# Kernel optimization log

Measured on AMD Instinct MI355X. Metric: run time of the kernel, lower is better.

The kernel has to match this reference:

```python
import jax, jax.numpy as jnp
import numpy as np

N = 25000   # nodes of type 'window'
E = 200000  # edges per relation
H = 512     # hidden_channels
OUT = 250   # out_channels
L = 4       # num_layers
R = 3       # relations: near, close, sim


def setup_inputs() -> dict:
    key = jax.random.key(0)
    ks = jax.random.split(key, 8)
    s = 1.0 / np.sqrt(H).astype(np.float32)
    x = jax.random.normal(ks[0], (N, H), jnp.float32)
    W_pre = jax.random.normal(ks[1], (H, H), jnp.float32) * s
    W_post = jax.random.normal(ks[2], (H, H), jnp.float32) * s
    Wl = jax.random.normal(ks[3], (L, R, H, H), jnp.float32) * s   # SAGEConv lin_l (neighbors)
    Wr = jax.random.normal(ks[4], (L, R, H, H), jnp.float32) * s   # SAGEConv lin_r (root)
    bl = jnp.zeros((L, R, H), jnp.float32)                         # lin_l bias
    W_out = jax.random.normal(ks[5], (H, OUT), jnp.float32) * s
    b_out = jnp.zeros((OUT,), jnp.float32)
    edges = jax.random.randint(ks[6], (R, 2, E), 0, N, jnp.int32)  # [rel, (src,dst), E]
    return dict(x=x, W_pre=W_pre, W_post=W_post, Wl=Wl, Wr=Wr, bl=bl,
                W_out=W_out, b_out=b_out, edges=edges)


def _leaky(v):
    return jnp.where(v >= 0, v, 0.2 * v)


def reference(x, W_pre, W_post, Wl, Wr, bl, W_out, b_out, edges):
    # pretransform + post_transform: leaky(leaky(x @ Wpre) @ Wpost)
    h = _leaky(_leaky(x @ W_pre) @ W_post)

    # per-relation destination in-degree (constant across layers)
    inv_deg = []
    for r in range(R):
        cnt = jax.ops.segment_sum(jnp.ones((E,), h.dtype), edges[r, 1], num_segments=N)
        inv_deg.append(1.0 / jnp.maximum(cnt, 1.0))  # [N]

    for l in range(L):
        acc = jnp.zeros_like(h)
        for r in range(R):
            src, dst = edges[r, 0], edges[r, 1]
            # mean aggregation of neighbor features over destinations
            agg = jax.ops.segment_sum(h[src], dst, num_segments=N) * inv_deg[r][:, None]
            # SAGEConv: lin_l(agg) + lin_r(x_root)
            acc = acc + (agg @ Wl[l, r] + bl[l, r] + h @ Wr[l, r])
        # HeteroConv aggr='mean' across relations, then LeakyReLU(0.2)
        h = _leaky(acc / R)

    return h @ W_out + b_out
```

## Files before the change

kernel.cpp:

```cpp
#include <hip/hip_runtime.h>

#define N_ 25000
#define E_ 200000
#define H_ 512
#define OUT_ 250
#define WSZ (H_ * H_)

typedef unsigned short u16;
typedef unsigned int u32;
typedef __bf16 bf16x8 __attribute__((ext_vector_type(8)));
typedef float f32x4 __attribute__((ext_vector_type(4)));

__device__ __forceinline__ u16 f2b(float f) {
  union { float f; u32 u; } c; c.f = f;
  u32 r = c.u + 0x7FFFu + ((c.u >> 16) & 1u);
  return (u16)(r >> 16);
}
__device__ __forceinline__ void async16(const void* g, void* l) {
  __builtin_amdgcn_global_load_lds((__attribute__((address_space(1))) void*)g,
                                   (__attribute__((address_space(3))) void*)l, 16, 0, 0);
}

__global__ void conv_hist(const float* __restrict__ x, u16* __restrict__ xb,
                          const int* __restrict__ edges, int* __restrict__ counts) {
  const int i = blockIdx.x * 256 + threadIdx.x;
  if (i < 3 * E_) {
    int r = i / E_, e = i - r * E_;
    int dst = edges[r * 2 * E_ + E_ + e];
    atomicAdd(&counts[r * N_ + dst], 1);
  }
  if (i < N_ * 512 / 4) {
    const float4 v = *(const float4*)(x + (size_t)i * 4);
    ushort4 o;
    o.x = f2b(v.x); o.y = f2b(v.y); o.z = f2b(v.z); o.w = f2b(v.w);
    *(ushort4*)(xb + (size_t)i * 4) = o;
  }
}

__global__ void prep_all(const float* __restrict__ Wpre, const float* __restrict__ Wpost,
                         const float* __restrict__ Wl, const float* __restrict__ Wr,
                         const float* __restrict__ Wout, const float* __restrict__ bl,
                         const float* __restrict__ bout,
                         u16* __restrict__ WT, u16* __restrict__ WoutT,
                         float* __restrict__ blSum, float* __restrict__ bOutF) {
  __shared__ u16 tile[32][33];
  const int id = blockIdx.z;
  const int tx = blockIdx.x, ty = blockIdx.y;
  const int x = threadIdx.x, y = threadIdx.y;
  if (id == 19) {
    if (tx || ty) return;
    const int t = y * 32 + x;
    for (int t0 = t; t0 < 512; t0 += 256) {
      for (int l = 0; l < 4; ++l)
        blSum[l * 512 + t0] = bl[(l * 3 + 0) * 512 + t0] + bl[(l * 3 + 1) * 512 + t0] +
                              bl[(l * 3 + 2) * 512 + t0];
    }
    if (t < 256) bOutF[t] = (t < OUT_) ? bout[t] : 0.0f;
    return;
  }
  if (id == 18) {
    if (tx >= 8) return;
#pragma unroll
    for (int i = 0; i < 4; ++i) {
      int row = ty * 32 + y + i * 8;
      int col = tx * 32 + x;
      tile[y + i * 8][x] = (col < OUT_) ? f2b(Wout[(size_t)row * OUT_ + col]) : (u16)0;
    }
    __syncthreads();
#pragma unroll
    for (int i = 0; i < 4; ++i)
      WoutT[(tx * 32 + y + i * 8) * 512 + ty * 32 + x] = tile[x][y + i * 8];
    return;
  }
  const float* src = nullptr;
  bool sum3 = false;
  if (id == 0) src = Wpre;
  else if (id == 1) src = Wpost;
  else {
    int li = (id - 2) >> 2, ri = (id - 2) & 3;
    if (ri < 3) src = Wl + (size_t)(li * 3 + ri) * WSZ;
    else { sum3 = true; src = Wr + (size_t)(li * 3) * WSZ; }
  }
#pragma unroll
  for (int i = 0; i < 4; ++i) {
    int row = ty * 32 + y + i * 8;
    int col = tx * 32 + x;
    float f = src[(size_t)row * 512 + col];
    if (sum3) f += src[WSZ + (size_t)row * 512 + col] + src[2 * WSZ + (size_t)row * 512 + col];
    tile[y + i * 8][x] = f2b(f);
  }
  __syncthreads();
#pragma unroll
  for (int i = 0; i < 4; ++i)
    WT[(size_t)id * WSZ + (tx * 32 + y + i * 8) * 512 + ty * 32 + x] = tile[x][y + i * 8];
}

__global__ __launch_bounds__(1024) void scan_kernel(const int* __restrict__ counts,
                                                    int* __restrict__ rowptr,
                                                    int* __restrict__ cursor,
                                                    float* __restrict__ invdeg) {
  const int r = blockIdx.x;
  const int* cnt = counts + r * N_;
  int* rp = rowptr + r * (N_ + 1);
  int* cur = cursor + r * N_;
  __shared__ int wsum[2][16];
  const int tid = threadIdx.x;
  const int wv = tid >> 6, lane = tid & 63;
  int roff = 0;
  int par = 0;
  for (int base = 0; base < N_; base += 1024, par ^= 1) {
    int v = (base + tid < N_) ? cnt[base + tid] : 0;
    int inc = v;
#pragma unroll
    for (int d = 1; d < 64; d <<= 1) {
      int t = __shfl_up(inc, d, 64);
      if (lane >= d) inc += t;
    }
    if (lane == 63) wsum[par][wv] = inc;
    __syncthreads();
    if (tid < 16) {
      int s = wsum[par][tid];
#pragma unroll
      for (int d = 1; d < 16; d <<= 1) {
        int t = __shfl_up(s, d, 64);
        if (tid >= d) s += t;
      }
      wsum[par][tid] = s;
    }
    __syncthreads();
    int woff = (wv == 0) ? 0 : wsum[par][wv - 1];
    int excl = roff + woff + inc - v;
    if (base + tid < N_) {
      rp[base + tid] = excl; cur[base + tid] = excl;
      invdeg[r * N_ + base + tid] = 1.0f / fmaxf((float)v, 1.0f);
    }
    roff += wsum[par][15];
  }
  if (tid == 0) rp[N_] = roff;
}

__global__ void scatter_kernel(const int* __restrict__ edges, int* __restrict__ cursor,
                               int* __restrict__ colidx) {
  int idx = blockIdx.x * 256 + threadIdx.x;
  if (idx >= 3 * E_) return;
  int r = idx / E_, e = idx - r * E_;
  int src = edges[r * 2 * E_ + e];
  int dst = edges[r * 2 * E_ + E_ + e];
  int pos = atomicAdd(&cursor[r * N_ + dst], 1);
  colidx[r * E_ + pos] = src;
}

__device__ __forceinline__ void acc8(float* acc, uint4 u) {
  union { u32 u; float f; } c;
  c.u = u.x << 16;          acc[0] += c.f;
  c.u = u.x & 0xffff0000u;  acc[1] += c.f;
  c.u = u.y << 16;          acc[2] += c.f;
  c.u = u.y & 0xffff0000u;  acc[3] += c.f;
  c.u = u.z << 16;          acc[4] += c.f;
  c.u = u.z & 0xffff0000u;  acc[5] += c.f;
  c.u = u.w << 16;          acc[6] += c.f;
  c.u = u.w & 0xffff0000u;  acc[7] += c.f;
}

__global__ __launch_bounds__(256) void agg_kernel(const u16* __restrict__ h,
                                                  const int* __restrict__ rowptr,
                                                  const int* __restrict__ colidx,
                                                  const float* __restrict__ invdeg,
                                                  u16* __restrict__ agg) {
  const int chunk = blockIdx.x & 7;
  const int nb = blockIdx.x >> 3;
  const int r = blockIdx.y;
  const int wv = threadIdx.x >> 6;
  const int lane = threadIdx.x & 63;
  const int grp = lane >> 3, sub = lane & 7;
  const int node = nb * 32 + wv * 8 + grp;
  if (node >= N_) return;
  const int* rp = rowptr + r * (N_ + 1);
  const int* ci = colidx + r * E_;
  const u16* hb = h + chunk * 64 + sub * 8;
  const int s = rp[node], e = rp[node + 1];
  float acc[8] = {0.f, 0.f, 0.f, 0.f, 0.f, 0.f, 0.f, 0.f};
  int p = s;
  for (; p + 4 <= e; p += 4) {
    int s0 = ci[p], s1 = ci[p + 1], s2 = ci[p + 2], s3 = ci[p + 3];
    uint4 u0 = *(const uint4*)(hb + (size_t)s0 * 512);
    uint4 u1 = *(const uint4*)(hb + (size_t)s1 * 512);
    uint4 u2 = *(const uint4*)(hb + (size_t)s2 * 512);
    uint4 u3 = *(const uint4*)(hb + (size_t)s3 * 512);
    acc8(acc, u0); acc8(acc, u1); acc8(acc, u2); acc8(acc, u3);
  }
  for (; p < e; ++p) acc8(acc, *(const uint4*)(hb + (size_t)ci[p] * 512));
  const float sc = invdeg[r * N_ + node];
  uint4 o;
  o.x = (u32)f2b(acc[0] * sc) | ((u32)f2b(acc[1] * sc) << 16);
  o.y = (u32)f2b(acc[2] * sc) | ((u32)f2b(acc[3] * sc) << 16);
  o.z = (u32)f2b(acc[4] * sc) | ((u32)f2b(acc[5] * sc) << 16);
  o.w = (u32)f2b(acc[6] * sc) | ((u32)f2b(acc[7] * sc) << 16);
  *(uint4*)(agg + ((size_t)r * N_ + node) * 512 + chunk * 64 + sub * 8) = o;
}

#define BM 128
#define BN 128
#define BK 64
#define CSTRIDE 136
__global__ __launch_bounds__(256, 4) void gemm_mfma(
    const u16* __restrict__ A0, const u16* __restrict__ A1,
    const u16* __restrict__ A2, const u16* __restrict__ A3,
    const u16* __restrict__ Bt, const float* __restrict__ bias,
    u16* __restrict__ C, float* __restrict__ Cf,
    int M, int G, int ldc, int Nreal, float scale, int leaky) {
  __shared__ __align__(16) u16 shmem[BM * CSTRIDE];
  u16* As = shmem;
  u16* Bs = shmem + BM * BK;
  const int tid = threadIdx.x;
  const int lane = tid & 63;
  const int w = tid >> 6;

  const int gx = gridDim.x;
  const int lin = blockIdx.y * gx + blockIdx.x;
  const int gsz = gx * 8;
  const int grp = lin / gsz;
  const int l = lin - grp * gsz;
  const int rem = (int)gridDim.y - grp * 8;
  int by, bx;
  if (rem >= 8) { by = grp * 8 + (l & 7); bx = l >> 3; }
  else          { by = grp * 8 + l % rem; bx = l / rem; }
  const int row0 = by * BM;
  const int col0 = bx * BN;

  int aOff[4], bOff[4], lOff[4];
#pragma unroll
  for (int i = 0; i < 4; ++i) {
    const int idx = i * 256 + tid;
    const int arow = idx >> 3;
    const int c = (idx & 7) ^ (arow & 7);
    int grow = row0 + arow; if (grow >= M) grow = M - 1;
    aOff[i] = grow * 512 + c * 8;
    bOff[i] = (col0 + arow) * 512 + c * 8;
    lOff[i] = idx * 16;
  }

  const int lm = lane & 15;
  const int lk = lane >> 4;
  const int x0 = ((lk ^ (lane & 7)) << 3);
  const int x1 = (((4 + lk) ^ (lane & 7)) << 3);
  const int wm = (w >> 1) * 64;
  const int wn = (w & 1) * 64;
  int aRow[4], bRow[4];
#pragma unroll
  for (int i = 0; i < 4; ++i) {
    aRow[i] = (wm + i * 16 + lm) * BK;
    bRow[i] = (wn + i * 16 + lm) * BK;
  }

  f32x4 acc[4][4] = {};

  for (int g = 0; g < G; ++g) {
    const u16* Ag = (g == 0) ? A0 : (g == 1) ? A1 : (g == 2) ? A2 : A3;
    const u16* Bg = Bt + ((size_t)g << 18);
#pragma unroll
    for (int ki = 0; ki < 8; ++ki) {
      const u16* Ab = Ag + ki * 64;
      const u16* Bb = Bg + ki * 64;
#pragma unroll
      for (int i = 0; i < 4; ++i) {
        async16(Ab + aOff[i], (char*)As + lOff[i]);
        async16(Bb + bOff[i], (char*)Bs + lOff[i]);
      }
      __syncthreads();
      {
        bf16x8 af[4], bfr[4];
#pragma unroll
        for (int i = 0; i < 4; ++i) {
          af[i]  = *(const bf16x8*)((const char*)As + ((aRow[i] + x0) << 1));
          bfr[i] = *(const bf16x8*)((const char*)Bs + ((bRow[i] + x0) << 1));
        }
#pragma unroll
        for (int i = 0; i < 4; ++i)
#pragma unroll
          for (int j = 0; j < 4; ++j)
            acc[i][j] = __builtin_amdgcn_mfma_f32_16x16x32_bf16(af[i], bfr[j], acc[i][j], 0, 0, 0);
#pragma unroll
        for (int i = 0; i < 4; ++i) {
          af[i]  = *(const bf16x8*)((const char*)As + ((aRow[i] + x1) << 1));
          bfr[i] = *(const bf16x8*)((const char*)Bs + ((bRow[i] + x1) << 1));
        }
#pragma unroll
        for (int i = 0; i < 4; ++i)
#pragma unroll
          for (int j = 0; j < 4; ++j)
            acc[i][j] = __builtin_amdgcn_mfma_f32_16x16x32_bf16(af[i], bfr[j], acc[i][j], 0, 0, 0);
      }
      __syncthreads();
    }
  }

  if (Cf) {
    const int crow_base = row0 + wm + (lk << 2);
    const int ccol_base = col0 + wn + lm;
#pragma unroll
    for (int i = 0; i < 4; ++i) {
#pragma unroll
      for (int j = 0; j < 4; ++j) {
        const int ccol = ccol_base + j * 16;
        const float badd = bias ? bias[ccol] : 0.0f;
#pragma unroll
        for (int rg = 0; rg < 4; ++rg) {
          const int crow = crow_base + i * 16 + rg;
          if (crow < M && ccol < Nreal) {
            float v = (acc[i][j][rg] + badd) * scale;
            if (leaky) v = (v >= 0.0f) ? v : 0.2f * v;
            Cf[(size_t)crow * ldc + ccol] = v;
          }
        }
      }
    }
    return;
  }
  {
    const int lrow_base = wm + (lk << 2);
    const int lcol_base = wn + lm;
#pragma unroll
    for (int i = 0; i < 4; ++i) {
#pragma unroll
      for (int j = 0; j < 4; ++j) {
        const int lcol = lcol_base + j * 16;
        const float badd = bias ? bias[col0 + lcol] : 0.0f;
#pragma unroll
        for (int rg = 0; rg < 4; ++rg) {
          const int lrow = lrow_base + i * 16 + rg;
          float v = (acc[i][j][rg] + badd) * scale;
          if (leaky) v = (v >= 0.0f) ? v : 0.2f * v;
          shmem[lrow * CSTRIDE + lcol] = f2b(v);
        }
      }
    }
    __syncthreads();
    const int rr = tid >> 4;
    const int c8 = (tid & 15) * 8;
#pragma unroll
    for (int pass = 0; pass < 8; ++pass) {
      const int r = pass * 16 + rr;
      const int crow = row0 + r;
      if (crow < M) {
        uint4 v = *(const uint4*)&shmem[r * CSTRIDE + c8];
        *(uint4*)(C + (size_t)crow * ldc + col0 + c8) = v;
      }
    }
  }
}

extern "C" void kernel_launch(void* const* d_in, const int* in_sizes, int n_in,
                              void* d_out, int out_size, void* d_ws, size_t ws_size,
                              hipStream_t stream) {
  const float* x     = (const float*)d_in[0];
  const float* Wpre  = (const float*)d_in[1];
  const float* Wpost = (const float*)d_in[2];
  const float* Wl    = (const float*)d_in[3];
  const float* Wr    = (const float*)d_in[4];
  const float* bl    = (const float*)d_in[5];
  const float* Wout  = (const float*)d_in[6];
  const float* bout  = (const float*)d_in[7];
  const int*   edges = (const int*)d_in[8];
  float* out = (float*)d_out;

  char* p = (char*)d_ws;
  auto alloc = [&](size_t b) { void* q = (void*)p; p += (b + 255) & ~(size_t)255; return q; };
  u16*   WT     = (u16*)alloc((size_t)18 * WSZ * 2);
  u16*   WoutT  = (u16*)alloc((size_t)256 * 512 * 2);
  float* blSum  = (float*)alloc(4 * 512 * 4);
  float* bOutF  = (float*)alloc(256 * 4);
  u16*   hA     = (u16*)alloc((size_t)N_ * 512 * 2);
  u16*   hB     = (u16*)alloc((size_t)N_ * 512 * 2);
  u16*   aggb   = (u16*)alloc((size_t)3 * N_ * 512 * 2);
  int*   counts = (int*)alloc(3 * N_ * 4);
  float* invdeg = (float*)alloc(3 * N_ * 4);
  int*   rowptr = (int*)alloc(3 * (N_ + 1) * 4);
  int*   cursor = (int*)alloc(3 * N_ * 4);
  int*   colidx = (int*)alloc((size_t)3 * E_ * 4);
  u16*   xb     = aggb;

  hipMemsetAsync(counts, 0, 3 * N_ * 4, stream);
  conv_hist<<<(N_ * 512 / 4 + 255) / 256, 256, 0, stream>>>(x, xb, edges, counts);
  prep_all<<<dim3(16, 16, 20), dim3(32, 8), 0, stream>>>(Wpre, Wpost, Wl, Wr, Wout, bl, bout,
                                                          WT, WoutT, blSum, bOutF);
  scan_kernel<<<3, 1024, 0, stream>>>(counts, rowptr, cursor, invdeg);
  scatter_kernel<<<(3 * E_ + 255) / 256, 256, 0, stream>>>(edges, cursor, colidx);

  const dim3 blk(256);
  const dim3 g512(512 / BN, (N_ + BM - 1) / BM);
  const dim3 gagg(((N_ + 31) / 32) * 8, 3);
  gemm_mfma<<<g512, blk, 0, stream>>>(xb, xb, xb, xb, WT, nullptr, hA, nullptr,
                                      N_, 1, 512, 512, 1.0f, 1);
  gemm_mfma<<<g512, blk, 0, stream>>>(hA, hA, hA, hA, WT + WSZ, nullptr, hB, nullptr,
                                      N_, 1, 512, 512, 1.0f, 1);

  u16* hc = hB; u16* hn = hA;
  for (int l = 0; l < 4; ++l) {
    agg_kernel<<<gagg, blk, 0, stream>>>(hc, rowptr, colidx, invdeg, aggb);
    gemm_mfma<<<g512, blk, 0, stream>>>(aggb, aggb + (size_t)N_ * 512, aggb + (size_t)2 * N_ * 512, hc,
                                        WT + (size_t)(2 + 4 * l) * WSZ, blSum + l * 512, hn, nullptr,
                                        N_, 4, 512, 512, 1.0f / 3.0f, 1);
    u16* t = hc; hc = hn; hn = t;
  }
  const dim3 gout(256 / BN, (N_ + BM - 1) / BM);
  gemm_mfma<<<gout, blk, 0, stream>>>(hc, hc, hc, hc, WoutT, bOutF, nullptr, out,
                                      N_, 1, OUT_, OUT_, 1.0f, 0);
}
```

Before: 792.2 us.

## Make aggregation persistent with per-XCC work queues and XCC-pinned column slices

The neighbor-aggregation kernel becomes a persistent kernel of 2048 blocks. Each block reads its hardware XCC id and uses it to pick which 64-column slice of h it gathers, so each die's L2 only ever holds one slice of the feature matrix. Node tiles for all three relations are handed out through a per-XCC atomic counter, one counter set per layer, to balance uneven in-degree work. This adds an atomic and two barriers per tile. Correctness relies on every XCC id 0–7 getting at least one block; if that fails, some column slices are never computed.

New measurement: 1.538 ms. +94.2%, slower.

```diff
diff --git a/kernel.cpp b/kernel.cpp
--- a/kernel.cpp
+++ b/kernel.cpp
@@ -162,41 +162,55 @@
   c.u = u.w & 0xffff0000u;  acc[7] += c.f;
 }
 
+#define AGG_TILES 782
+#define AGG_NT (AGG_TILES * 3)
 __global__ __launch_bounds__(256) void agg_kernel(const u16* __restrict__ h,
                                                   const int* __restrict__ rowptr,
                                                   const int* __restrict__ colidx,
                                                   const float* __restrict__ invdeg,
-                                                  u16* __restrict__ agg) {
-  const int chunk = blockIdx.x & 7;
-  const int nb = blockIdx.x >> 3;
-  const int r = blockIdx.y;
+                                                  u16* __restrict__ agg,
+                                                  int* __restrict__ wq) {
+  __shared__ int s_tile;
+  u32 xcc;
+  asm volatile("s_getreg_b32 %0, hwreg(HW_REG_XCC_ID)" : "=s"(xcc));
+  const int chunk = xcc & 7;
   const int wv = threadIdx.x >> 6;
   const int lane = threadIdx.x & 63;
   const int grp = lane >> 3, sub = lane & 7;
-  const int node = nb * 32 + wv * 8 + grp;
-  if (node >= N_) return;
-  const int* rp = rowptr + r * (N_ + 1);
-  const int* ci = colidx + r * E_;
   const u16* hb = h + chunk * 64 + sub * 8;
-  const int s = rp[node], e = rp[node + 1];
-  float acc[8] = {0.f, 0.f, 0.f, 0.f, 0.f, 0.f, 0.f, 0.f};
-  int p = s;
-  for (; p + 4 <= e; p += 4) {
-    int s0 = ci[p], s1 = ci[p + 1], s2 = ci[p + 2], s3 = ci[p + 3];
-    uint4 u0 = *(const uint4*)(hb + (size_t)s0 * 512);
-    uint4 u1 = *(const uint4*)(hb + (size_t)s1 * 512);
-    uint4 u2 = *(const uint4*)(hb + (size_t)s2 * 512);
-    uint4 u3 = *(const uint4*)(hb + (size_t)s3 * 512);
-    acc8(acc, u0); acc8(acc, u1); acc8(acc, u2); acc8(acc, u3);
-  }
-  for (; p < e; ++p) acc8(acc, *(const uint4*)(hb + (size_t)ci[p] * 512));
-  const float sc = invdeg[r * N_ + node];
-  uint4 o;
-  o.x = (u32)f2b(acc[0] * sc) | ((u32)f2b(acc[1] * sc) << 16);
-  o.y = (u32)f2b(acc[2] * sc) | ((u32)f2b(acc[3] * sc) << 16);
-  o.z = (u32)f2b(acc[4] * sc) | ((u32)f2b(acc[5] * sc) << 16);
-  o.w = (u32)f2b(acc[6] * sc) | ((u32)f2b(acc[7] * sc) << 16);
-  *(uint4*)(agg + ((size_t)r * N_ + node) * 512 + chunk * 64 + sub * 8) = o;
+  for (;;) {
+    if (threadIdx.x == 0) s_tile = atomicAdd(&wq[chunk], 1);
+    __syncthreads();
+    const int t = s_tile;
+    __syncthreads();
+    if (t >= AGG_NT) break;
+    const int r = t / AGG_TILES;
+    const int ti = t - r * AGG_TILES;
+    const int node = ti * 32 + wv * 8 + grp;
+    if (node < N_) {
+      const int* rp = rowptr + r * (N_ + 1);
+      const int* ci = colidx + r * E_;
+      const int s = rp[node], e = rp[node + 1];
+      float acc[8] = {0.f, 0.f, 0.f, 0.f, 0.f, 0.f, 0.f, 0.f};
+      int p = s;
+      for (; p + 4 <= e; p += 4) {
+        int s0 = ci[p], s1 = ci[p + 1], s2 = ci[p + 2], s3 = ci[p + 3];
+        uint4 u0 = *(const uint4*)(hb + (size_t)s0 * 512);
+        uint4 u1 = *(const uint4*)(hb + (size_t)s1 * 512);
+        uint4 u2 = *(const uint4*)(hb + (size_t)s2 * 512);
+        uint4 u3 = *(const uint4*)(hb + (size_t)s3 * 512);
+        acc8(acc, u0); acc8(acc, u1); acc8(acc, u2); acc8(acc, u3);
+      }
+      for (; p < e; ++p) acc8(acc, *(const uint4*)(hb + (size_t)ci[p] * 512));
+      const float sc = invdeg[r * N_ + node];
+      uint4 o;
+      o.x = (u32)f2b(acc[0] * sc) | ((u32)f2b(acc[1] * sc) << 16);
+      o.y = (u32)f2b(acc[2] * sc) | ((u32)f2b(acc[3] * sc) << 16);
+      o.z = (u32)f2b(acc[4] * sc) | ((u32)f2b(acc[5] * sc) << 16);
+      o.w = (u32)f2b(acc[6] * sc) | ((u32)f2b(acc[7] * sc) << 16);
+      *(uint4*)(agg + ((size_t)r * N_ + node) * 512 + chunk * 64 + sub * 8) = o;
+    }
+  }
 }
 
 #define BM 128
@@ -378,9 +392,11 @@
   int*   rowptr = (int*)alloc(3 * (N_ + 1) * 4);
   int*   cursor = (int*)alloc(3 * N_ * 4);
   int*   colidx = (int*)alloc((size_t)3 * E_ * 4);
+  int*   wq     = (int*)alloc(32 * 4);
   u16*   xb     = aggb;
 
   hipMemsetAsync(counts, 0, 3 * N_ * 4, stream);
+  hipMemsetAsync(wq, 0, 32 * 4, stream);
   conv_hist<<<(N_ * 512 / 4 + 255) / 256, 256, 0, stream>>>(x, xb, edges, counts);
   prep_all<<<dim3(16, 16, 20), dim3(32, 8), 0, stream>>>(Wpre, Wpost, Wl, Wr, Wout, bl, bout,
                                                           WT, WoutT, blSum, bOutF);
@@ -389,7 +405,6 @@
 
   const dim3 blk(256);
   const dim3 g512(512 / BN, (N_ + BM - 1) / BM);
-  const dim3 gagg(((N_ + 31) / 32) * 8, 3);
   gemm_mfma<<<g512, blk, 0, stream>>>(xb, xb, xb, xb, WT, nullptr, hA, nullptr,
                                       N_, 1, 512, 512, 1.0f, 1);
   gemm_mfma<<<g512, blk, 0, stream>>>(hA, hA, hA, hA, WT + WSZ, nullptr, hB, nullptr,
@@ -397,7 +412,7 @@
 
   u16* hc = hB; u16* hn = hA;
   for (int l = 0; l < 4; ++l) {
-    agg_kernel<<<gagg, blk, 0, stream>>>(hc, rowptr, colidx, invdeg, aggb);
+    agg_kernel<<<2048, blk, 0, stream>>>(hc, rowptr, colidx, invdeg, aggb, wq + l * 8);
     gemm_mfma<<<g512, blk, 0, stream>>>(aggb, aggb + (size_t)N_ * 512, aggb + (size_t)2 * N_ * 512, hc,
                                         WT + (size_t)(2 + 4 * l) * WSZ, blSum + l * 512, hn, nullptr,
                                         N_, 4, 512, 512, 1.0f / 3.0f, 1);
```
